# Optimization experiments

Measured on AMD Instinct MI355X. Metric: run time of the kernel, lower is better.

## Reference

```python
import jax, jax.numpy as jnp
import numpy as np

KINEMATIC_CHAIN = [[0,2,5,8,11],[0,1,4,7,10],[0,3,6,9,12,15],[9,14,17,19,21],[9,13,16,18,20]]
_paths = [c[1:] for c in KINEMATIC_CHAIN]
SEG_S = np.array([p[i] for p in _paths for i in range(len(p)-1)])      # [16] segment start joints
SEG_E = np.array([p[i+1] for p in _paths for i in range(len(p)-1)])    # [16] segment end joints
PATH_ID = np.array([k for k, p in enumerate(_paths) for _ in range(len(p)-1)])
N_PATHS = len(_paths)
P_ONEHOT = (PATH_ID[:, None] == np.arange(N_PATHS)[None, :]).astype(np.float32)  # [16,5]


def _safe_normalize(v):
    ss = jnp.sum(v * v, axis=-1, keepdims=True)
    return jnp.where(ss > 0, v / jnp.sqrt(jnp.where(ss > 0, ss, 1.0)), 0.0)


def _gli_pairwise(s1, e1, s2, e2):
    # all inputs broadcast to [..., 3]; returns Gauss linking integral per segment pair
    r13, r14 = s2 - s1, e2 - s1
    r23, r24 = s2 - e1, e2 - e1
    r12, r34 = e1 - s1, e2 - s2
    f0 = _safe_normalize(jnp.cross(r13, r14))
    f1 = _safe_normalize(jnp.cross(r14, r24))
    f2 = _safe_normalize(jnp.cross(r24, r23))
    f3 = _safe_normalize(jnp.cross(r23, r13))
    def asin_dot(a, b):
        return jnp.arcsin(jnp.clip(jnp.sum(a * b, -1), -1.0, 1.0))
    total = asin_dot(f0, f1) + asin_dot(f1, f2) + asin_dot(f2, f3) + asin_dot(f3, f0)
    sign = jnp.sum(jnp.cross(r34, r12) * r13, -1)
    mult = jnp.where(sign <= 0, -1.0, 1.0)
    return mult * total / (4.0 * jnp.pi)


def _bbox_xz(m):
    x, z = m[..., 0], m[..., 2]
    return x.min(-1), x.max(-1), z.min(-1), z.max(-1)


def setup_inputs() -> dict:
    key = jax.random.key(0)
    k1, k2 = jax.random.split(key)
    B, F, J = 64, 240, 22
    motion1 = jax.random.normal(k1, (B, F, J, 3), dtype=jnp.float32)
    motion2 = jax.random.normal(k2, (B, F, J, 3), dtype=jnp.float32)
    return {"motion1": motion1, "motion2": motion2}


def reference(motion1, motion2):
    B, F = motion1.shape[0], motion1.shape[1]
    P = jnp.asarray(P_ONEHOT, motion1.dtype)
    # gather all 16 skeleton segments, broadcast to 16x16 segment pairs
    s1 = motion1[..., SEG_S, :][..., :, None, :]   # [B,F,16,1,3]
    e1 = motion1[..., SEG_E, :][..., :, None, :]
    s2 = motion2[..., SEG_S, :][..., None, :, :]   # [B,F,1,16,3]
    e2 = motion2[..., SEG_E, :][..., None, :, :]
    gli_seg = _gli_pairwise(s1, e1, s2, e2)        # [B,F,16,16]
    # sum segment-pair GLIs into path-pair blocks -> [B,F,5,5]
    gli_pose = jnp.einsum('bfmn,mi,nj->bfij', gli_seg, P, P)

    # xz bounding-box overlap per frame, then dilate by 1 frame (window start-1..end+1)
    nx1, xx1, nz1, xz1 = _bbox_xz(motion1)
    nx2, xx2, nz2, xz2 = _bbox_xz(motion2)
    flag = (xx1 >= nx2) & (xx2 >= nx1) & (xz1 >= nz2) & (xz2 >= nz1)   # [B,F]
    pad = jnp.zeros_like(flag[:, :1])
    mask = flag | jnp.concatenate([flag[:, 1:], pad], 1) | jnp.concatenate([pad, flag[:, :-1]], 1)
    gli_motion = gli_pose * mask[..., None, None].astype(gli_pose.dtype)

    vel = jnp.abs(gli_motion[:, 1:] - gli_motion[:, :-1]).reshape(B, F - 1, -1)
    return vel.max(-1)
```

## Files before the change

kernel.cpp:

```cpp
#include <hip/hip_runtime.h>
#include <math.h>

#define BB 64
#define FF 240
#define NJ 22
#define NFRM (BB * FF)

#define PK8(a0,a1,a2,a3,a4,a5,a6,a7) \
  (  (unsigned long long)(a0)        | ((unsigned long long)(a1) << 5)  \
   | ((unsigned long long)(a2) << 10)| ((unsigned long long)(a3) << 15) \
   | ((unsigned long long)(a4) << 20)| ((unsigned long long)(a5) << 25) \
   | ((unsigned long long)(a6) << 30)| ((unsigned long long)(a7) << 35) )
static constexpr unsigned long long SEG_S_LO = PK8(2,5,8,1,4,7,3,6);
static constexpr unsigned long long SEG_S_HI = PK8(9,12,14,17,19,13,16,18);
static constexpr unsigned long long SEG_E_LO = PK8(5,8,11,4,7,10,6,9);
static constexpr unsigned long long SEG_E_HI = PK8(12,15,17,19,21,16,18,20);
static constexpr unsigned PO_PK = 0u | (3u<<5) | (6u<<10) | (10u<<15) | (13u<<20);
static constexpr unsigned PC_PK = 3u | (3u<<5) | (4u<<10) | (3u<<15)  | (3u<<20);

__device__ __forceinline__ int seg_start(int m){
    unsigned long long p = (m < 8) ? SEG_S_LO : SEG_S_HI;
    return (int)((p >> ((m & 7) * 5)) & 31);
}
__device__ __forceinline__ int seg_end(int m){
    unsigned long long p = (m < 8) ? SEG_E_LO : SEG_E_HI;
    return (int)((p >> ((m & 7) * 5)) & 31);
}

typedef float v2 __attribute__((ext_vector_type(2)));
__device__ __forceinline__ v2 vset(float a){ v2 r; r.x = a; r.y = a; return r; }
__device__ __forceinline__ v2 vfma(v2 a, v2 b, v2 c){ return __builtin_elementwise_fma(a, b, c); }

struct V3p { v2 x, y, z; };
__device__ __forceinline__ V3p subp(V3p a, V3p b){ return {a.x-b.x, a.y-b.y, a.z-b.z}; }
__device__ __forceinline__ V3p crsp(V3p a, V3p b){
    return { vfma(a.y, b.z, -(a.z*b.y)), vfma(a.z, b.x, -(a.x*b.z)), vfma(a.x, b.y, -(a.y*b.x)) };
}
__device__ __forceinline__ v2 dtp(V3p a, V3p b){ return vfma(a.x, b.x, vfma(a.y, b.y, a.z*b.z)); }
__device__ __forceinline__ v2 clamp1p(v2 d){
    return __builtin_elementwise_min(__builtin_elementwise_max(d, vset(-1.0f)), vset(1.0f));
}
__device__ __forceinline__ v2 asin_fast2(v2 d){
    v2 ax = __builtin_elementwise_abs(d);
    v2 p = vfma(vfma(vfma(vset(-0.0187293f), ax, vset(0.0742610f)), ax, vset(-0.2121144f)),
                ax, vset(1.5707288f));
    v2 om = vset(1.0f) - ax;
    v2 s; s.x = __builtin_amdgcn_sqrtf(om.x); s.y = __builtin_amdgcn_sqrtf(om.y);
    v2 r = vset(1.57079632679f) - s * p;
    return __builtin_elementwise_copysign(r, d);
}

__global__ void __launch_bounds__(256) k_main(const float* __restrict__ m1,
                                              const float* __restrict__ m2,
                                              float* __restrict__ gp,
                                              int* __restrict__ flags){
    __shared__ __align__(8) float pts[4][2][136];
    __shared__ float g[4][2][256];
    __shared__ float ext[4][2][8];
    int tid = threadIdx.x;
    int w = tid >> 6, lane = tid & 63;
    int fr0 = blockIdx.x * 8 + w * 2;

    const float2* gs1 = (const float2*)(m1 + (size_t)fr0 * 66);
    const float2* gs2 = (const float2*)(m2 + (size_t)fr0 * 66);
    for (int u = lane; u < 132; u += 64){
        bool a = u < 66;
        int v = a ? u : u - 66;
        ((float2*)pts[w][a ? 0 : 1])[v] = (a ? gs1 : gs2)[v];
    }
    __syncthreads();

    if (lane < 16){
        int f = lane >> 3;
        int sel = lane & 7;
        int mot = sel >> 2;
        int c = sel & 2;
        bool mx = sel & 1;
        const float* P = &pts[w][mot][f * 66];
        float a = 1e30f;
        #pragma unroll
        for (int j = 0; j < NJ; ++j){
            float v = P[j*3 + c];
            a = fminf(a, mx ? -v : v);
        }
        ext[w][f][sel] = mx ? -a : a;
    }

    int n = lane & 15, q = lane >> 4;
    const float* P1 = pts[w][0];
    const float* P2 = pts[w][1];
    int js2 = seg_start(n) * 3, je2 = seg_end(n) * 3;
    V3p s2 = { v2{P2[js2  ], P2[66+js2  ]},
               v2{P2[js2+1], P2[66+js2+1]},
               v2{P2[js2+2], P2[66+js2+2]} };
    V3p e2 = { v2{P2[je2  ], P2[66+je2  ]},
               v2{P2[je2+1], P2[66+je2+1]},
               v2{P2[je2+2], P2[66+je2+2]} };

    v2 rd01[4], rd12[4], rd23[4], rd30[4];
    v2 q01[4], q12[4], q23[4], q30[4];
    v2 sg[4];
    #pragma unroll
    for (int k = 0; k < 4; ++k){
        int m = q + 4 * k;
        int js1 = seg_start(m) * 3, je1 = seg_end(m) * 3;
        V3p s1 = { v2{P1[js1  ], P1[66+js1  ]},
                   v2{P1[js1+1], P1[66+js1+1]},
                   v2{P1[js1+2], P1[66+js1+2]} };
        V3p e1 = { v2{P1[je1  ], P1[66+je1  ]},
                   v2{P1[je1+1], P1[66+je1+1]},
                   v2{P1[je1+2], P1[66+je1+2]} };
        V3p r13 = subp(s2, s1), r14 = subp(e2, s1);
        V3p r23 = subp(s2, e1), r24 = subp(e2, e1);
        V3p f0 = crsp(r13, r14);
        V3p f1 = crsp(r14, r24);
        V3p f2 = crsp(r24, r23);
        V3p f3 = crsp(r23, r13);
        v2 ss0 = dtp(f0,f0), ss1 = dtp(f1,f1), ss2 = dtp(f2,f2), ss3 = dtp(f3,f3);
        rd01[k] = dtp(f0,f1); rd12[k] = dtp(f1,f2);
        rd23[k] = dtp(f2,f3); rd30[k] = dtp(f3,f0);
        q01[k] = ss0*ss1; q12[k] = ss1*ss2; q23[k] = ss2*ss3; q30[k] = ss3*ss0;
        sg[k] = dtp(f3, r14);
    }
    v2 i01[4], i12[4], i23[4], i30[4];
    #pragma unroll
    for (int k = 0; k < 4; ++k){
        i01[k].x = rsqrtf(fmaxf(q01[k].x, 1e-30f));
        i01[k].y = rsqrtf(fmaxf(q01[k].y, 1e-30f));
        i12[k].x = rsqrtf(fmaxf(q12[k].x, 1e-30f));
        i12[k].y = rsqrtf(fmaxf(q12[k].y, 1e-30f));
        i23[k].x = rsqrtf(fmaxf(q23[k].x, 1e-30f));
        i23[k].y = rsqrtf(fmaxf(q23[k].y, 1e-30f));
        i30[k].x = rsqrtf(fmaxf(q30[k].x, 1e-30f));
        i30[k].y = rsqrtf(fmaxf(q30[k].y, 1e-30f));
    }
    #pragma unroll
    for (int k = 0; k < 4; ++k){
        v2 t = asin_fast2(clamp1p(rd01[k] * i01[k]))
             + asin_fast2(clamp1p(rd12[k] * i12[k]))
             + asin_fast2(clamp1p(rd23[k] * i23[k]))
             + asin_fast2(clamp1p(rd30[k] * i30[k]));
        float r0 = (sg[k].x >= 0.0f ? -t.x : t.x) * 0.07957747154594767f;
        float r1 = (sg[k].y >= 0.0f ? -t.y : t.y) * 0.07957747154594767f;
        g[w][0][(k << 6) | lane] = r0;
        g[w][1][(k << 6) | lane] = r1;
    }
    __syncthreads();

    if (lane < 50){
        int f = lane >= 25 ? 1 : 0;
        int pp = lane - f * 25;
        int i = pp / 5, j = pp - i * 5;
        int poi = (int)((PO_PK >> (i*5)) & 31), pci = (int)((PC_PK >> (i*5)) & 31);
        int poj = (int)((PO_PK >> (j*5)) & 31), pcj = (int)((PC_PK >> (j*5)) & 31);
        float s = 0.0f;
        for (int a = 0; a < pci; ++a)
            for (int b = 0; b < pcj; ++b)
                s += g[w][f][(poi + a) * 16 + (poj + b)];
        gp[(size_t)(fr0 + f) * 25 + pp] = s;
    } else if (lane < 52){
        int f = lane - 50;
        const float* e = ext[w][f];
        flags[fr0 + f] = (e[1] >= e[4] && e[5] >= e[0] &&
                          e[3] >= e[6] && e[7] >= e[2]) ? 1 : 0;
    }
}

__global__ void __launch_bounds__(256) k_vel(const float* __restrict__ gp,
                                             const int* __restrict__ flags,
                                             float* __restrict__ out){
    int idx = blockIdx.x * blockDim.x + threadIdx.x;
    const int total = BB * (FF - 1);
    if (idx >= total) return;
    int b = idx / (FF - 1);
    int f = idx - b * (FF - 1);
    const int* fl = flags + b * FF;

    int v0 = fl[f] | fl[f + 1];
    if (f > 0) v0 |= fl[f - 1];
    float mk0 = v0 ? 1.0f : 0.0f;

    int v1 = fl[f] | fl[f + 1];
    if (f + 2 < FF) v1 |= fl[f + 2];
    float mk1 = v1 ? 1.0f : 0.0f;

    const float* g0 = gp + (size_t)(b * FF + f) * 25;
    const float* g1 = g0 + 25;
    float mx = 0.0f;
    #pragma unroll
    for (int p = 0; p < 25; ++p){
        float d = fabsf(g1[p] * mk1 - g0[p] * mk0);
        mx = fmaxf(mx, d);
    }
    out[idx] = mx;
}

extern "C" void kernel_launch(void* const* d_in, const int* in_sizes, int n_in,
                              void* d_out, int out_size, void* d_ws, size_t ws_size,
                              hipStream_t stream) {
    const float* m1 = (const float*)d_in[0];
    const float* m2 = (const float*)d_in[1];
    float* gp    = (float*)d_ws;
    int*   flags = (int*)((char*)d_ws + (size_t)NFRM * 25 * 4);
    float* out = (float*)d_out;

    k_main<<<NFRM / 8, 256, 0, stream>>>(m1, m2, gp, flags);
    k_vel<<<(BB * (FF - 1) + 255) / 256, 256, 0, stream>>>(gp, flags, out);
}
```

Baseline: 75.76 us.

## Fuse GLI and velocity kernels using per-block halo frame recomputation

Merges the main GLI kernel and the velocity/max kernel into one launch. Each block recomputes the GLI matrix for one halo frame past its 8-frame tile, and the bbox flags for neighbouring frames, so the frame differences and dilated mask can be done in shared memory. This removes the workspace round-trip and the second launch. In exchange each block does about 1/8 extra GLI work, plus uncoalesced global loads for the halo frame and extents.

```diff
diff --git a/kernel.cpp b/kernel.cpp
--- a/kernel.cpp
+++ b/kernel.cpp
@@ -27,10 +27,42 @@
     return (int)((p >> ((m & 7) * 5)) & 31);
 }
 
+struct F3 { float x, y, z; };
+__device__ __forceinline__ F3 sub(F3 a, F3 b){ return {a.x-b.x, a.y-b.y, a.z-b.z}; }
+__device__ __forceinline__ F3 crs(F3 a, F3 b){
+    return {fmaf(a.y, b.z, -a.z*b.y), fmaf(a.z, b.x, -a.x*b.z), fmaf(a.x, b.y, -a.y*b.x)};
+}
+__device__ __forceinline__ float dt(F3 a, F3 b){ return fmaf(a.x, b.x, fmaf(a.y, b.y, a.z*b.z)); }
+__device__ __forceinline__ float clamp1(float d){ return fminf(fmaxf(d, -1.0f), 1.0f); }
+__device__ __forceinline__ float asin_fast(float d){
+    float ax = fabsf(d);
+    float p = fmaf(fmaf(fmaf(-0.0187293f, ax, 0.0742610f), ax, -0.2121144f), ax, 1.5707288f);
+    float r = 1.57079632679f - __builtin_amdgcn_sqrtf(1.0f - ax) * p;
+    return copysignf(r, d);
+}
+__device__ __forceinline__ float gli_scalar(F3 s1, F3 e1, F3 s2, F3 e2){
+    F3 r13 = sub(s2, s1), r14 = sub(e2, s1);
+    F3 r23 = sub(s2, e1), r24 = sub(e2, e1);
+    F3 f0 = crs(r13, r14);
+    F3 f1 = crs(r14, r24);
+    F3 f2 = crs(r24, r23);
+    F3 f3 = crs(r23, r13);
+    float ss0 = dt(f0,f0), ss1 = dt(f1,f1), ss2 = dt(f2,f2), ss3 = dt(f3,f3);
+    float i01 = rsqrtf(fmaxf(ss0*ss1, 1e-30f));
+    float i12 = rsqrtf(fmaxf(ss1*ss2, 1e-30f));
+    float i23 = rsqrtf(fmaxf(ss2*ss3, 1e-30f));
+    float i30 = rsqrtf(fmaxf(ss3*ss0, 1e-30f));
+    float t = asin_fast(clamp1(dt(f0,f1) * i01))
+            + asin_fast(clamp1(dt(f1,f2) * i12))
+            + asin_fast(clamp1(dt(f2,f3) * i23))
+            + asin_fast(clamp1(dt(f3,f0) * i30));
+    float sg = dt(f3, r14);
+    return (sg >= 0.0f ? -t : t) * 0.07957747154594767f;
+}
+
 typedef float v2 __attribute__((ext_vector_type(2)));
 __device__ __forceinline__ v2 vset(float a){ v2 r; r.x = a; r.y = a; return r; }
 __device__ __forceinline__ v2 vfma(v2 a, v2 b, v2 c){ return __builtin_elementwise_fma(a, b, c); }
-
 struct V3p { v2 x, y, z; };
 __device__ __forceinline__ V3p subp(V3p a, V3p b){ return {a.x-b.x, a.y-b.y, a.z-b.z}; }
 __device__ __forceinline__ V3p crsp(V3p a, V3p b){
@@ -50,23 +82,47 @@
     return __builtin_elementwise_copysign(r, d);
 }
 
-__global__ void __launch_bounds__(256) k_main(const float* __restrict__ m1,
-                                              const float* __restrict__ m2,
-                                              float* __restrict__ gp,
-                                              int* __restrict__ flags){
+__global__ void __launch_bounds__(256) k_fused(const float* __restrict__ m1,
+                                               const float* __restrict__ m2,
+                                               float* __restrict__ out){
     __shared__ __align__(8) float pts[4][2][136];
-    __shared__ float g[4][2][256];
-    __shared__ float ext[4][2][8];
+    __shared__ float g2[4][2][256];
+    __shared__ float gh[256];
+    __shared__ float gpL[9][25];
+    __shared__ float extL[11][8];
+    __shared__ int   flagsL[11];
     int tid = threadIdx.x;
     int w = tid >> 6, lane = tid & 63;
-    int fr0 = blockIdx.x * 8 + w * 2;
-
-    const float2* gs1 = (const float2*)(m1 + (size_t)fr0 * 66);
-    const float2* gs2 = (const float2*)(m2 + (size_t)fr0 * 66);
+    int fr0 = blockIdx.x * 8;
+    int fl0 = fr0 % FF;
+    bool haloValid = (fl0 != 232);
+    bool prevValid = (fl0 != 0);
+    int frA = fr0 + w * 2;
+
+    const float2* gs1 = (const float2*)(m1 + (size_t)frA * 66);
+    const float2* gs2 = (const float2*)(m2 + (size_t)frA * 66);
     for (int u = lane; u < 132; u += 64){
         bool a = u < 66;
         int v = a ? u : u - 66;
         ((float2*)pts[w][a ? 0 : 1])[v] = (a ? gs1 : gs2)[v];
+    }
+    if (w == 0 && lane >= 40){
+        int sel3 = lane - 40;
+        int which = sel3 >> 3;
+        int sel = sel3 & 7;
+        int frX = (which == 0) ? (fr0 - 1) : (fr0 + 7 + which);
+        frX = max(0, min(frX, NFRM - 1));
+        int mot = sel >> 2;
+        int c = sel & 2;
+        bool mx = sel & 1;
+        const float* P = (mot ? m2 : m1) + (size_t)frX * 66;
+        float a = 1e30f;
+        #pragma unroll
+        for (int j = 0; j < NJ; ++j){
+            float v = P[j*3 + c];
+            a = fminf(a, mx ? -v : v);
+        }
+        extL[(which == 0) ? 0 : (9 + which - 1)][sel] = mx ? -a : a;
     }
     __syncthreads();
 
@@ -83,67 +139,81 @@
             float v = P[j*3 + c];
             a = fminf(a, mx ? -v : v);
         }
-        ext[w][f][sel] = mx ? -a : a;
+        extL[1 + 2*w + f][sel] = mx ? -a : a;
     }
 
     int n = lane & 15, q = lane >> 4;
-    const float* P1 = pts[w][0];
-    const float* P2 = pts[w][1];
-    int js2 = seg_start(n) * 3, je2 = seg_end(n) * 3;
-    V3p s2 = { v2{P2[js2  ], P2[66+js2  ]},
-               v2{P2[js2+1], P2[66+js2+1]},
-               v2{P2[js2+2], P2[66+js2+2]} };
-    V3p e2 = { v2{P2[je2  ], P2[66+je2  ]},
-               v2{P2[je2+1], P2[66+je2+1]},
-               v2{P2[je2+2], P2[66+je2+2]} };
-
-    v2 rd01[4], rd12[4], rd23[4], rd30[4];
-    v2 q01[4], q12[4], q23[4], q30[4];
-    v2 sg[4];
-    #pragma unroll
-    for (int k = 0; k < 4; ++k){
-        int m = q + 4 * k;
-        int js1 = seg_start(m) * 3, je1 = seg_end(m) * 3;
-        V3p s1 = { v2{P1[js1  ], P1[66+js1  ]},
-                   v2{P1[js1+1], P1[66+js1+1]},
-                   v2{P1[js1+2], P1[66+js1+2]} };
-        V3p e1 = { v2{P1[je1  ], P1[66+je1  ]},
-                   v2{P1[je1+1], P1[66+je1+1]},
-                   v2{P1[je1+2], P1[66+je1+2]} };
-        V3p r13 = subp(s2, s1), r14 = subp(e2, s1);
-        V3p r23 = subp(s2, e1), r24 = subp(e2, e1);
-        V3p f0 = crsp(r13, r14);
-        V3p f1 = crsp(r14, r24);
-        V3p f2 = crsp(r24, r23);
-        V3p f3 = crsp(r23, r13);
-        v2 ss0 = dtp(f0,f0), ss1 = dtp(f1,f1), ss2 = dtp(f2,f2), ss3 = dtp(f3,f3);
-        rd01[k] = dtp(f0,f1); rd12[k] = dtp(f1,f2);
-        rd23[k] = dtp(f2,f3); rd30[k] = dtp(f3,f0);
-        q01[k] = ss0*ss1; q12[k] = ss1*ss2; q23[k] = ss2*ss3; q30[k] = ss3*ss0;
-        sg[k] = dtp(f3, r14);
-    }
-    v2 i01[4], i12[4], i23[4], i30[4];
-    #pragma unroll
-    for (int k = 0; k < 4; ++k){
-        i01[k].x = rsqrtf(fmaxf(q01[k].x, 1e-30f));
-        i01[k].y = rsqrtf(fmaxf(q01[k].y, 1e-30f));
-        i12[k].x = rsqrtf(fmaxf(q12[k].x, 1e-30f));
-        i12[k].y = rsqrtf(fmaxf(q12[k].y, 1e-30f));
-        i23[k].x = rsqrtf(fmaxf(q23[k].x, 1e-30f));
-        i23[k].y = rsqrtf(fmaxf(q23[k].y, 1e-30f));
-        i30[k].x = rsqrtf(fmaxf(q30[k].x, 1e-30f));
-        i30[k].y = rsqrtf(fmaxf(q30[k].y, 1e-30f));
-    }
-    #pragma unroll
-    for (int k = 0; k < 4; ++k){
-        v2 t = asin_fast2(clamp1p(rd01[k] * i01[k]))
-             + asin_fast2(clamp1p(rd12[k] * i12[k]))
-             + asin_fast2(clamp1p(rd23[k] * i23[k]))
-             + asin_fast2(clamp1p(rd30[k] * i30[k]));
-        float r0 = (sg[k].x >= 0.0f ? -t.x : t.x) * 0.07957747154594767f;
-        float r1 = (sg[k].y >= 0.0f ? -t.y : t.y) * 0.07957747154594767f;
-        g[w][0][(k << 6) | lane] = r0;
-        g[w][1][(k << 6) | lane] = r1;
+    {
+        const float* P1 = pts[w][0];
+        const float* P2 = pts[w][1];
+        int js2 = seg_start(n) * 3, je2 = seg_end(n) * 3;
+        V3p s2 = { v2{P2[js2  ], P2[66+js2  ]},
+                   v2{P2[js2+1], P2[66+js2+1]},
+                   v2{P2[js2+2], P2[66+js2+2]} };
+        V3p e2 = { v2{P2[je2  ], P2[66+je2  ]},
+                   v2{P2[je2+1], P2[66+je2+1]},
+                   v2{P2[je2+2], P2[66+je2+2]} };
+        v2 rd01[4], rd12[4], rd23[4], rd30[4];
+        v2 q01[4], q12[4], q23[4], q30[4];
+        v2 sg[4];
+        #pragma unroll
+        for (int k = 0; k < 4; ++k){
+            int m = q + 4 * k;
+            int js1 = seg_start(m) * 3, je1 = seg_end(m) * 3;
+            V3p s1 = { v2{P1[js1  ], P1[66+js1  ]},
+                       v2{P1[js1+1], P1[66+js1+1]},
+                       v2{P1[js1+2], P1[66+js1+2]} };
+            V3p e1 = { v2{P1[je1  ], P1[66+je1  ]},
+                       v2{P1[je1+1], P1[66+je1+1]},
+                       v2{P1[je1+2], P1[66+je1+2]} };
+            V3p r13 = subp(s2, s1), r14 = subp(e2, s1);
+            V3p r23 = subp(s2, e1), r24 = subp(e2, e1);
+            V3p f0 = crsp(r13, r14);
+            V3p f1 = crsp(r14, r24);
+            V3p f2 = crsp(r24, r23);
+            V3p f3 = crsp(r23, r13);
+            v2 ss0 = dtp(f0,f0), ss1 = dtp(f1,f1), ss2 = dtp(f2,f2), ss3 = dtp(f3,f3);
+            rd01[k] = dtp(f0,f1); rd12[k] = dtp(f1,f2);
+            rd23[k] = dtp(f2,f3); rd30[k] = dtp(f3,f0);
+            q01[k] = ss0*ss1; q12[k] = ss1*ss2; q23[k] = ss2*ss3; q30[k] = ss3*ss0;
+            sg[k] = dtp(f3, r14);
+        }
+        v2 i01[4], i12[4], i23[4], i30[4];
+        #pragma unroll
+        for (int k = 0; k < 4; ++k){
+            i01[k].x = rsqrtf(fmaxf(q01[k].x, 1e-30f));
+            i01[k].y = rsqrtf(fmaxf(q01[k].y, 1e-30f));
+            i12[k].x = rsqrtf(fmaxf(q12[k].x, 1e-30f));
+            i12[k].y = rsqrtf(fmaxf(q12[k].y, 1e-30f));
+            i23[k].x = rsqrtf(fmaxf(q23[k].x, 1e-30f));
+            i23[k].y = rsqrtf(fmaxf(q23[k].y, 1e-30f));
+            i30[k].x = rsqrtf(fmaxf(q30[k].x, 1e-30f));
+            i30[k].y = rsqrtf(fmaxf(q30[k].y, 1e-30f));
+        }
+        #pragma unroll
+        for (int k = 0; k < 4; ++k){
+            v2 t = asin_fast2(clamp1p(rd01[k] * i01[k]))
+                 + asin_fast2(clamp1p(rd12[k] * i12[k]))
+                 + asin_fast2(clamp1p(rd23[k] * i23[k]))
+                 + asin_fast2(clamp1p(rd30[k] * i30[k]));
+            float r0 = (sg[k].x >= 0.0f ? -t.x : t.x) * 0.07957747154594767f;
+            float r1 = (sg[k].y >= 0.0f ? -t.y : t.y) * 0.07957747154594767f;
+            g2[w][0][(k << 6) | lane] = r0;
+            g2[w][1][(k << 6) | lane] = r1;
+        }
+    }
+    {
+        int frH = min(fr0 + 8, NFRM - 1);
+        int mh = tid >> 4, nh = tid & 15;
+        const float* P1g = m1 + (size_t)frH * 66;
+        const float* P2g = m2 + (size_t)frH * 66;
+        int ja = seg_start(mh) * 3, jb = seg_end(mh) * 3;
+        int jc = seg_start(nh) * 3, jd = seg_end(nh) * 3;
+        F3 s1 = {P1g[ja], P1g[ja+1], P1g[ja+2]};
+        F3 e1 = {P1g[jb], P1g[jb+1], P1g[jb+2]};
+        F3 s2 = {P2g[jc], P2g[jc+1], P2g[jc+2]};
+        F3 e2 = {P2g[jd], P2g[jd+1], P2g[jd+2]};
+        gh[mh * 16 + nh] = gli_scalar(s1, e1, s2, e2);
     }
     __syncthreads();
 
@@ -156,43 +226,46 @@
         float s = 0.0f;
         for (int a = 0; a < pci; ++a)
             for (int b = 0; b < pcj; ++b)
-                s += g[w][f][(poi + a) * 16 + (poj + b)];
-        gp[(size_t)(fr0 + f) * 25 + pp] = s;
-    } else if (lane < 52){
-        int f = lane - 50;
-        const float* e = ext[w][f];
-        flags[fr0 + f] = (e[1] >= e[4] && e[5] >= e[0] &&
-                          e[3] >= e[6] && e[7] >= e[2]) ? 1 : 0;
-    }
-}
-
-__global__ void __launch_bounds__(256) k_vel(const float* __restrict__ gp,
-                                             const int* __restrict__ flags,
-                                             float* __restrict__ out){
-    int idx = blockIdx.x * blockDim.x + threadIdx.x;
-    const int total = BB * (FF - 1);
-    if (idx >= total) return;
-    int b = idx / (FF - 1);
-    int f = idx - b * (FF - 1);
-    const int* fl = flags + b * FF;
-
-    int v0 = fl[f] | fl[f + 1];
-    if (f > 0) v0 |= fl[f - 1];
-    float mk0 = v0 ? 1.0f : 0.0f;
-
-    int v1 = fl[f] | fl[f + 1];
-    if (f + 2 < FF) v1 |= fl[f + 2];
-    float mk1 = v1 ? 1.0f : 0.0f;
-
-    const float* g0 = gp + (size_t)(b * FF + f) * 25;
-    const float* g1 = g0 + 25;
-    float mx = 0.0f;
-    #pragma unroll
-    for (int p = 0; p < 25; ++p){
-        float d = fabsf(g1[p] * mk1 - g0[p] * mk0);
-        mx = fmaxf(mx, d);
-    }
-    out[idx] = mx;
+                s += g2[w][f][(poi + a) * 16 + (poj + b)];
+        gpL[2*w + f][pp] = s;
+    } else {
+        int h = w * 14 + (lane - 50);
+        if (h < 25){
+            int pp = h;
+            int i = pp / 5, j = pp - i * 5;
+            int poi = (int)((PO_PK >> (i*5)) & 31), pci = (int)((PC_PK >> (i*5)) & 31);
+            int poj = (int)((PO_PK >> (j*5)) & 31), pcj = (int)((PC_PK >> (j*5)) & 31);
+            float s = 0.0f;
+            for (int a = 0; a < pci; ++a)
+                for (int b = 0; b < pcj; ++b)
+                    s += gh[(poi + a) * 16 + (poj + b)];
+            gpL[8][pp] = s;
+        } else if (h < 36){
+            int i = h - 25;
+            const float* e = extL[i];
+            int ok = (e[1] >= e[4] && e[5] >= e[0] &&
+                      e[3] >= e[6] && e[7] >= e[2]) ? 1 : 0;
+            bool valid = (i == 0) ? prevValid : (i <= 8 ? true : haloValid);
+            flagsL[i] = valid ? ok : 0;
+        }
+    }
+    __syncthreads();
+
+    if (tid < 8 && !(tid == 7 && !haloValid)){
+        int m0 = flagsL[tid] | flagsL[tid+1] | flagsL[tid+2];
+        int m1f = flagsL[tid+1] | flagsL[tid+2] | flagsL[tid+3];
+        float mk0 = m0 ? 1.0f : 0.0f;
+        float mk1 = m1f ? 1.0f : 0.0f;
+        const float* a0 = gpL[tid];
+        const float* a1 = gpL[tid+1];
+        float mx = 0.0f;
+        #pragma unroll
+        for (int p = 0; p < 25; ++p){
+            float d = fabsf(a1[p] * mk1 - a0[p] * mk0);
+            mx = fmaxf(mx, d);
+        }
+        out[(size_t)(fr0 / FF) * (FF - 1) + fl0 + tid] = mx;
+    }
 }
 
 extern "C" void kernel_launch(void* const* d_in, const int* in_sizes, int n_in,
@@ -200,10 +273,7 @@
                               hipStream_t stream) {
     const float* m1 = (const float*)d_in[0];
     const float* m2 = (const float*)d_in[1];
-    float* gp    = (float*)d_ws;
-    int*   flags = (int*)((char*)d_ws + (size_t)NFRM * 25 * 4);
     float* out = (float*)d_out;
-
-    k_main<<<NFRM / 8, 256, 0, stream>>>(m1, m2, gp, flags);
-    k_vel<<<(BB * (FF - 1) + 255) / 256, 256, 0, stream>>>(gp, flags, out);
-}
+    (void)d_ws; (void)ws_size;
+    k_fused<<<NFRM / 8, 256, 0, stream>>>(m1, m2, out);
+}
```

Result: no change. 77.16 us (+1.8%).
